# Performance work log

Measured on AMD Instinct MI355X. Metric: run time of the kernel, lower is better.

## Reference

```python
import jax, jax.numpy as jnp
import numpy as np

TIME_STEPS = 50
LEFT_PAD = 250 // TIME_STEPS            # 5
MAX_DELAY = LEFT_PAD if LEFT_PAD % 2 == 1 else LEFT_PAD + 1  # 5 (odd)
SIG = float(MAX_DELAY // 2)             # 2.0, frozen
CIN = 34 * 34 * 2                       # 2312
HID = 300
NOUT = 10
BETA = 0.9
THRESH = 1.0
BATCH = 128


def setup_inputs() -> dict:
    key = jax.random.key(0)
    k = jax.random.split(key, 6)
    data = jax.random.normal(k[0], (BATCH, TIME_STEPS, CIN), jnp.float32)
    W1 = jax.random.normal(k[1], (HID, CIN), jnp.float32) / np.sqrt(CIN * MAX_DELAY).astype(np.float32)
    P1 = jax.random.uniform(k[2], (HID, CIN), jnp.float32, -SIG, SIG)
    b1 = jnp.zeros((HID,), jnp.float32)
    W2 = jax.random.normal(k[3], (NOUT, HID), jnp.float32) / np.sqrt(HID * MAX_DELAY).astype(np.float32)
    P2 = jax.random.uniform(k[4], (NOUT, HID), jnp.float32, -SIG, SIG)
    b2 = jnp.zeros((NOUT,), jnp.float32)
    return {"data": data, "W1": W1, "P1": P1, "b1": b1, "W2": W2, "P2": P2, "b2": b2}


def make_gauss_kernel(W, P):
    # DCLS 'gauss': weight W placed at learnable position P (centered at KS//2)
    # with Gaussian of width SIG, normalized over the KS taps. kernel_count=1.
    idx = jnp.arange(MAX_DELAY, dtype=W.dtype)              # [KS]
    c = P[..., None] + (MAX_DELAY // 2)                     # [O, I, 1]
    g = jnp.exp(-0.5 * ((idx - c) / SIG) ** 2)              # [O, I, KS]
    g = g / (g.sum(-1, keepdims=True) + 1e-7)
    return W[..., None] * g                                 # [O, I, KS]


def delay_conv(x, W, P, b):
    # x: [B, Cin, L], valid conv with synthesized kernel -> [B, Cout, L-KS+1]
    K = make_gauss_kernel(W, P)
    y = jax.lax.conv_general_dilated(x, K, window_strides=(1,), padding='VALID',
                                     dimension_numbers=('NCH', 'OIH', 'NCH'))
    return y + b[None, :, None]


def lif_scan(x):
    # snntorch Leaky (reset-by-subtraction, reset detached):
    #   mem_t = beta*mem_{t-1} + x_t - H(mem_{t-1}-thr)*thr ;  spk_t = H(mem_t-thr)
    # x: [B, C, T] -> (spk [T,B,C], mem [T,B,C])
    def step(mem, xt):
        reset = (mem > THRESH).astype(xt.dtype)
        mem_new = BETA * mem + xt - reset * THRESH
        spk = (mem_new > THRESH).astype(xt.dtype)
        return mem_new, (spk, mem_new)

    xs = jnp.moveaxis(x, 2, 0)                              # [T, B, C]
    mem0 = jnp.zeros(x.shape[:2], x.dtype)
    _, (spks, mems) = jax.lax.scan(step, mem0, xs)
    return spks, mems


def reference(data, W1, P1, b1, W2, P2, b2):
    # pad time (dim -2) on the left, permute to [B, Cin, T+pad]
    x = jnp.pad(data, ((0, 0), (LEFT_PAD, 0), (0, 0)))
    x = jnp.transpose(x, (0, 2, 1))                         # [B, CIN, T+pad]
    x = delay_conv(x, W1, P1, b1)                           # [B, HID, T1]
    spk1, _ = lif_scan(x)                                   # [T1, B, HID]
    h = jnp.moveaxis(spk1, 0, 2)                            # [B, HID, T1]
    h = jnp.pad(h, ((0, 0), (0, 0), (LEFT_PAD, 0)))
    y = delay_conv(h, W2, P2, b2)                           # [B, NOUT, T2]
    spk2, mem2 = lif_scan(y)                                # [T2, B, NOUT] each
    return spk2, mem2
```

## Files before the change

### kernel.cpp

```cpp
#include <hip/hip_runtime.h>

#define BSZ  128
#define TT   50
#define CIN  2312
#define HID  300
#define NOUT 10
#define KS   5
#define T1   51
#define T2   52

#define NC32 73
#define KFRAG_U 20480

typedef unsigned int u32;
typedef unsigned short u16;
typedef __attribute__((ext_vector_type(8))) short s16x8;
typedef __attribute__((ext_vector_type(4))) float f32x4;

#define EK1f 0.88249690258459546f
#define EK2f 0.60653065971263342f
#define EK3f 0.32465246735834974f
#define EK4f 0.13533528323661270f

static __device__ __forceinline__ u16 bfhi(float x) {
  u32 u = __float_as_uint(x);
  return (u16)((u + 0x7fffu + ((u >> 16) & 1u)) >> 16);
}
static __device__ __forceinline__ float bf2f(u16 h) {
  return __uint_as_float(((u32)h) << 16);
}

__global__ __launch_bounds__(256) void snn_prepm(
    const float* __restrict__ W1, const float* __restrict__ P1,
    u16* __restrict__ K1bf)
{
  const int c  = blockIdx.x;
  const int ow = blockIdx.y;
  const int tid = threadIdx.x;
  const int nt = tid >> 6, ll = tid & 63;
  const int g = ll >> 4, lr = ll & 15;
  const int o  = ow * 64 + nt * 16 + lr;
  const int ib = c * 32 + g * 8;

  s16x8 hv[5], lv[5];
#pragma unroll
  for (int k = 0; k < 5; ++k)
#pragma unroll
    for (int j = 0; j < 8; ++j) { hv[k][j] = 0; lv[k][j] = 0; }

  if (o < HID) {
    const float* wrow = W1 + (size_t)o * CIN;
    const float* prow = P1 + (size_t)o * CIN;
#pragma unroll
    for (int j = 0; j < 8; ++j) {
      const int i = ib + j;
      if (i < CIN) {
        const float w1 = wrow[i], p1 = prow[i];
        const float cc = p1 + 2.0f;
        const float E0 = __expf(-0.125f * cc * cc);
        const float U  = __expf(0.25f * cc);
        const float u2 = U * U;
        const float e0 = E0;
        const float e1 = E0 * U * EK1f;
        const float e2 = E0 * u2 * EK2f;
        const float e3 = E0 * (u2 * U) * EK3f;
        const float e4 = E0 * (u2 * u2) * EK4f;
        const float inv = 1.0f / (((((e0 + e1) + e2) + e3) + e4) + 1e-7f);
        const float vk[5] = { w1 * (e0 * inv), w1 * (e1 * inv),
                              w1 * (e2 * inv), w1 * (e3 * inv),
                              w1 * (e4 * inv) };
#pragma unroll
        for (int k = 0; k < 5; ++k) {
          const u16 h = bfhi(vk[k]);
          const u16 lo = bfhi(vk[k] - bf2f(h));
          hv[k][j] = (short)h; lv[k][j] = (short)lo;
        }
      }
    }
  }
  u16* base = K1bf + ((size_t)ow * NC32 + c) * KFRAG_U + nt * 1024 + ll * 8;
#pragma unroll
  for (int k = 0; k < 5; ++k) {
    *(s16x8*)(base + k * 4096)       = hv[k];
    *(s16x8*)(base + k * 4096 + 512) = lv[k];
  }
}

__global__ __launch_bounds__(256, 2) void snn_l1m(
    const float* __restrict__ data, const u16* __restrict__ K1bf,
    const float* __restrict__ b1v, u32* __restrict__ gbits)
{
  __shared__ double dsm[3264];
  u16* A16 = (u16*)dsm;

  const int tid = threadIdx.x;
  const int bid = blockIdx.x;
  const int rnk = (bid & 7) * 80 + (bid >> 3);
  const int ow = rnk >> 7;
  const int b  = rnk & 127;

  const int w  = tid >> 6, l = tid & 63;
  const int lr = l & 15, lg = l >> 4;

  const float* dbase = data + (size_t)b * (TT * CIN);
  const u16* kbw = K1bf + (size_t)ow * NC32 * KFRAG_U + w * 1024 + l * 8;

  const int s1 = tid >> 2;
  const int j4 = tid & 3;
  const int tp = s1 - 5;
  const bool avld = (tp >= 0) && (tp < TT);
  const float* aptr = dbase + (size_t)(avld ? tp : 0) * CIN + j4 * 8;

  if (tid < 64) {
    s16x8 z;
#pragma unroll
    for (int j = 0; j < 8; ++j) z[j] = 0;
    const int r = tid >> 4, sub = tid & 15;
    const int row = 64 + (sub >> 2), off = (sub & 3) * 8;
    *(s16x8*)(A16 + (r >> 1) * 5440 + (r & 1) * 2720 + row * 40 + off) = z;
  }

  s16x8 bh0[5], bl0[5], bh1[5], bl1[5];

#define ISSUE_B(DH, DL, CC)                                                   \
  {                                                                           \
    const u16* cb_ = kbw + (size_t)(CC) * KFRAG_U;                            \
    _Pragma("unroll")                                                         \
    for (int k = 0; k < 5; ++k) {                                             \
      DH[k] = *(const s16x8*)(cb_ + k * 4096);                                \
      DL[k] = *(const s16x8*)(cb_ + k * 4096 + 512);                          \
    }                                                                         \
  }

#define STAGE_A(CC)                                                           \
  {                                                                           \
    const float f_[8] = { ra0.x, ra0.y, ra0.z, ra0.w,                         \
                          ra1.x, ra1.y, ra1.z, ra1.w };                       \
    s16x8 hv_, lv_;                                                           \
    _Pragma("unroll")                                                         \
    for (int j = 0; j < 8; ++j) {                                             \
      const u16 h_ = bfhi(f_[j]);                                             \
      hv_[j] = (short)h_;                                                     \
      lv_[j] = (short)bfhi(f_[j] - bf2f(h_));                                 \
    }                                                                         \
    u16* bn_ = A16 + (((CC) + 1) & 1) * 5440;                                 \
    const int woff_ = s1 * 40 + ((j4 * 8) ^ ((s1 & 3) << 3));                 \
    *(s16x8*)(bn_ + woff_) = hv_;                                             \
    *(s16x8*)(bn_ + 2720 + woff_) = lv_;                                      \
    const int cn_ = ((CC) + 2 <= 72) ? (CC) + 2 : 72;                         \
    const bool iv_ = avld && ((cn_ < 72) || (j4 == 0));                       \
    const float* pp_ = aptr + (size_t)cn_ * 32;                               \
    ra0 = iv_ ? *(const float4*)(pp_)     : make_float4(0.f, 0.f, 0.f, 0.f);  \
    ra1 = iv_ ? *(const float4*)(pp_ + 4) : make_float4(0.f, 0.f, 0.f, 0.f);  \
  }

#define COMPUTE(BH, BL, CC)                                                   \
  {                                                                           \
    const u16* bc_ = A16 + ((CC) & 1) * 5440;                                 \
    _Pragma("unroll")                                                         \
    for (int k = 0; k < 5; ++k) {                                             \
      const int xk_ = ((lr + k) & 3) << 3;                                    \
      const int a0_ = (lr + k) * 40 + ((lg * 8) ^ xk_);                       \
      _Pragma("unroll")                                                       \
      for (int m = 0; m < 4; ++m) {                                           \
        const s16x8 ah_ = *(const s16x8*)(bc_ + a0_ + m * 640);               \
        const s16x8 al_ = *(const s16x8*)(bc_ + 2720 + a0_ + m * 640);        \
        accf[m] = __builtin_amdgcn_mfma_f32_16x16x32_bf16(ah_, BH[k], accf[m], 0, 0, 0); \
        accf[m] = __builtin_amdgcn_mfma_f32_16x16x32_bf16(al_, BH[k], accf[m], 0, 0, 0); \
        accf[m] = __builtin_amdgcn_mfma_f32_16x16x32_bf16(ah_, BL[k], accf[m], 0, 0, 0); \
      }                                                                       \
    }                                                                         \
  }

#define PROMOTE()                                                             \
  _Pragma("unroll")                                                           \
  for (int m = 0; m < 4; ++m)                                                 \
    _Pragma("unroll")                                                         \
    for (int q = 0; q < 4; ++q) {                                             \
      accd[m][q] += (double)accf[m][q];                                       \
      accf[m][q] = 0.f;                                                       \
    }

  f32x4 accf[4];
  double accd[4][4];
#pragma unroll
  for (int m = 0; m < 4; ++m)
#pragma unroll
    for (int q = 0; q < 4; ++q) { accf[m][q] = 0.f; accd[m][q] = 0.0; }

  ISSUE_B(bh0, bl0, 0);
  float4 ra0, ra1;
  ra0 = avld ? *(const float4*)(aptr)     : make_float4(0.f, 0.f, 0.f, 0.f);
  ra1 = avld ? *(const float4*)(aptr + 4) : make_float4(0.f, 0.f, 0.f, 0.f);
  {
    const float f_[8] = { ra0.x, ra0.y, ra0.z, ra0.w,
                          ra1.x, ra1.y, ra1.z, ra1.w };
    s16x8 hv_, lv_;
#pragma unroll
    for (int j = 0; j < 8; ++j) {
      const u16 h_ = bfhi(f_[j]);
      hv_[j] = (short)h_;
      lv_[j] = (short)bfhi(f_[j] - bf2f(h_));
    }
    const int woff_ = s1 * 40 + ((j4 * 8) ^ ((s1 & 3) << 3));
    *(s16x8*)(A16 + woff_) = hv_;
    *(s16x8*)(A16 + 2720 + woff_) = lv_;
  }
  {
    const float* pp_ = aptr + 32;
    ra0 = avld ? *(const float4*)(pp_)     : make_float4(0.f, 0.f, 0.f, 0.f);
    ra1 = avld ? *(const float4*)(pp_ + 4) : make_float4(0.f, 0.f, 0.f, 0.f);
  }
  __syncthreads();

  for (int pr = 0; pr < 36; ++pr) {
    const int c0 = 2 * pr, c1 = c0 + 1;
    ISSUE_B(bh1, bl1, c0 + 1);
    STAGE_A(c0);
    COMPUTE(bh0, bl0, c0);
    __syncthreads();
    ISSUE_B(bh0, bl0, c1 + 1);
    STAGE_A(c1);
    COMPUTE(bh1, bl1, c1);
    PROMOTE();
    __syncthreads();
  }
  COMPUTE(bh0, bl0, 72);
  PROMOTE();
  __syncthreads();

#undef ISSUE_B
#undef STAGE_A
#undef COMPUTE
#undef PROMOTE

  double* y1s = dsm;
#pragma unroll
  for (int m = 0; m < 4; ++m)
#pragma unroll
    for (int q = 0; q < 4; ++q) {
      const int t = 16 * m + lg * 4 + q;
      if (t < T1) y1s[t * 64 + 16 * w + lr] = accd[m][q];
    }
  __syncthreads();

  if (tid < 64) {
    const int o = ow * 64 + tid;
    const bool valid = o < HID;
    const double bias = valid ? (double)b1v[o] : 0.0;
    u32* bits = gbits + (size_t)b * 510;
    double mem = 0.0;
    for (int t = 0; t < T1; ++t) {
      const double x = y1s[t * 64 + tid] + bias;
      const double reset = (mem > 1.0) ? 1.0 : 0.0;
      mem = __dsub_rn(__dadd_rn(__dmul_rn(0.9, mem), x), reset);
      const unsigned long long mk = __ballot(valid && (mem > 1.0));
      if (tid == 0)  bits[t * 10 + 2 * ow]     = (u32)mk;
      if (tid == 32) bits[t * 10 + 2 * ow + 1] = (u32)(mk >> 32);
    }
  }
}

__device__ __forceinline__ void layer1_tile_g(
    int b, int ow, int tid,
    const float* __restrict__ data, const float* __restrict__ W1,
    const float* __restrict__ P1, const float* __restrict__ b1v,
    double* __restrict__ dsm, u32* __restrict__ bits)
{
  float* Bsf = (float*)dsm;
  float* As  = (float*)dsm + 2880;

  const int ty = tid >> 5;
  const int tx = tid & 31;
  const int r0 = ty << 3;
  const int c0 = tx << 1;

  const float* abase = data + (size_t)b * (TT * CIN);

  const int slot = tid >> 2;
  const int pair = tid & 3;
  const int tp   = slot - 5;

  const int isub = tid & 7;
  const int oA = tid >> 3;
  const int oB = oA + 32;
  const int boA = ow * 64 + oA;
  const int boB = ow * 64 + oB;
  const bool vB = boB < HID;

  double acc[8][2];
#pragma unroll
  for (int r = 0; r < 8; ++r) { acc[r][0] = 0.0; acc[r][1] = 0.0; }

  float2 aA = make_float2(0.f, 0.f);
  float wA = 0.f, pA = 0.f, wB = 0.f, pB = 0.f;
  if (tid < 220 && tp >= 0)
    aA = *(const float2*)(abase + (size_t)tp * CIN + 2 * pair);
  wA = W1[(size_t)boA * CIN + isub];
  pA = P1[(size_t)boA * CIN + isub];
  if (vB) {
    wB = W1[(size_t)boB * CIN + isub];
    pB = P1[(size_t)boB * CIN + isub];
  }

  for (int i0 = 0; i0 < CIN; i0 += 8) {
    if (tid < 220) {
      As[(2 * pair) * 80 + slot]     = aA.x;
      As[(2 * pair + 1) * 80 + slot] = aA.y;
    }
    {
      const float c  = pA + 2.0f;
      const float E0 = __expf(-0.125f * c * c);
      const float U  = __expf(0.25f * c);
      const float u2 = U * U;
      const float e0 = E0;
      const float e1 = E0 * U * EK1f;
      const float e2 = E0 * u2 * EK2f;
      const float e3 = E0 * (u2 * U) * EK3f;
      const float e4 = E0 * (u2 * u2) * EK4f;
      const float inv = 1.0f / (((((e0 + e1) + e2) + e3) + e4) + 1e-7f);
      float* bp = Bsf + isub * 72 + oA;
      bp[0]    = wA * (e0 * inv);
      bp[576]  = wA * (e1 * inv);
      bp[1152] = wA * (e2 * inv);
      bp[1728] = wA * (e3 * inv);
      bp[2304] = wA * (e4 * inv);
    }
    {
      const float c  = pB + 2.0f;
      const float E0 = __expf(-0.125f * c * c);
      const float U  = __expf(0.25f * c);
      const float u2 = U * U;
      const float e0 = E0;
      const float e1 = E0 * U * EK1f;
      const float e2 = E0 * u2 * EK2f;
      const float e3 = E0 * (u2 * U) * EK3f;
      const float e4 = E0 * (u2 * u2) * EK4f;
      const float inv = 1.0f / (((((e0 + e1) + e2) + e3) + e4) + 1e-7f);
      float* bp = Bsf + isub * 72 + oB;
      bp[0]    = wB * (e0 * inv);
      bp[576]  = wB * (e1 * inv);
      bp[1152] = wB * (e2 * inv);
      bp[1728] = wB * (e3 * inv);
      bp[2304] = wB * (e4 * inv);
    }
    __syncthreads();

    const int i0n = i0 + 8;
    if (i0n < CIN) {
      if (tid < 220 && tp >= 0)
        aA = *(const float2*)(abase + (size_t)tp * CIN + i0n + 2 * pair);
      wA = W1[(size_t)boA * CIN + i0n + isub];
      pA = P1[(size_t)boA * CIN + i0n + isub];
      if (vB) {
        wB = W1[(size_t)boB * CIN + i0n + isub];
        pB = P1[(size_t)boB * CIN + i0n + isub];
      }
    }

    float accf[8][2];
#pragma unroll
    for (int r = 0; r < 8; ++r) { accf[r][0] = 0.f; accf[r][1] = 0.f; }
#pragma unroll
    for (int kk = 0; kk < 8; ++kk) {
      const float* ap = &As[kk * 80 + r0];
      const float4 a0 = *(const float4*)(ap);
      const float4 a1 = *(const float4*)(ap + 4);
      const float4 a2 = *(const float4*)(ap + 8);
      float av[12];
      av[0] = a0.x; av[1] = a0.y; av[2]  = a0.z; av[3]  = a0.w;
      av[4] = a1.x; av[5] = a1.y; av[6]  = a1.z; av[7]  = a1.w;
      av[8] = a2.x; av[9] = a2.y; av[10] = a2.z; av[11] = a2.w;
      float bv[KS][2];
#pragma unroll
      for (int k = 0; k < KS; ++k) {
        const float2 bb = *(const float2*)&Bsf[(k * 8 + kk) * 72 + c0];
        bv[k][0] = bb.x; bv[k][1] = bb.y;
      }
#pragma unroll
      for (int k = 0; k < KS; ++k)
#pragma unroll
        for (int r = 0; r < 8; ++r) {
          accf[r][0] = fmaf(av[r + k], bv[k][0], accf[r][0]);
          accf[r][1] = fmaf(av[r + k], bv[k][1], accf[r][1]);
        }
    }
#pragma unroll
    for (int r = 0; r < 8; ++r) {
      acc[r][0] += (double)accf[r][0];
      acc[r][1] += (double)accf[r][1];
    }
    __syncthreads();
  }

  double* y1s = dsm;
#pragma unroll
  for (int r = 0; r < 8; ++r) {
    const int t = r0 + r;
    if (t < T1) {
      y1s[t * 64 + c0]     = acc[r][0];
      y1s[t * 64 + c0 + 1] = acc[r][1];
    }
  }
  __syncthreads();

  if (tid < 64) {
    const int o = ow * 64 + tid;
    const bool valid = o < HID;
    const double bias = valid ? (double)b1v[o] : 0.0;
    double mem = 0.0;
    for (int t = 0; t < T1; ++t) {
      const double x = y1s[t * 64 + tid] + bias;
      const double reset = (mem > 1.0) ? 1.0 : 0.0;
      mem = __dsub_rn(__dadd_rn(__dmul_rn(0.9, mem), x), reset);
      const unsigned long long mk = __ballot(valid && (mem > 1.0));
      if (tid == 0)  bits[t * 10 + 2 * ow]     = (u32)mk;
      if (tid == 32) bits[t * 10 + 2 * ow + 1] = (u32)(mk >> 32);
    }
  }
  __syncthreads();
}

__device__ __forceinline__ void layer2_lif2(
    int b, int tid, float* smem,
    const float* __restrict__ W2, const float* __restrict__ P2,
    const float* __restrict__ b2, float* __restrict__ out)
{
  float* K2s = smem;
  const u32* lbits = (const u32*)(smem + 15000);
  float* y2s = smem + 15510;

  for (int idx = tid; idx < NOUT * HID; idx += 256) {
    const int o = idx / HID, i = idx % HID;
    const float w = W2[idx], p = P2[idx];
    const float c = p + 2.0f;
    float e[KS], s = 0.f;
#pragma unroll
    for (int k = 0; k < KS; ++k) {
      const float d = ((float)k - c) * 0.5f;
      e[k] = __expf(-0.5f * d * d);
      s += e[k];
    }
    const float denom = s + 1e-7f;
#pragma unroll
    for (int k = 0; k < KS; ++k)
      K2s[(o * KS + k) * HID + i] = w * (e[k] / denom);
  }
  __syncthreads();

  for (int task = tid; task < T2 * NOUT; task += 256) {
    const int t2 = task / NOUT, o = task % NOUT;
    float acc = b2[o];
#pragma unroll
    for (int k = 0; k < KS; ++k) {
      const int tp = t2 + k - KS;
      if (tp < 0 || tp >= T1) continue;
      const float* kr = K2s + (o * KS + k) * HID;
      const u32* br = lbits + tp * 10;
      for (int i = 0; i < HID; ++i)
        acc = fmaf((float)((br[i >> 5] >> (i & 31)) & 1u), kr[i], acc);
    }
    y2s[task] = acc;
  }
  __syncthreads();

  if (tid < NOUT) {
    float mem = 0.f;
    for (int t = 0; t < T2; ++t) {
      const float x = y2s[t * NOUT + tid];
      const float reset = (mem > 1.0f) ? 1.0f : 0.0f;
      mem = __fsub_rn(__fadd_rn(__fmul_rn(0.9f, mem), x), reset);
      out[(size_t)t * (BSZ * NOUT) + b * NOUT + tid] = (mem > 1.0f) ? 1.0f : 0.0f;
      out[(size_t)T2 * BSZ * NOUT + (size_t)t * (BSZ * NOUT) + b * NOUT + tid] = mem;
    }
  }
}

__global__ __launch_bounds__(256) void snn_l1(
    const float* __restrict__ data, const float* __restrict__ W1,
    const float* __restrict__ P1, const float* __restrict__ b1v,
    u32* __restrict__ gbits)
{
  __shared__ double dsm[3264];
  const int ow = blockIdx.x, b = blockIdx.y;
  layer1_tile_g(b, ow, threadIdx.x, data, W1, P1, b1v, dsm,
                gbits + (size_t)b * 510);
}

__global__ __launch_bounds__(256) void snn_l2k(
    const u32* __restrict__ gbits,
    const float* __restrict__ W2, const float* __restrict__ P2,
    const float* __restrict__ b2, float* __restrict__ out)
{
  __shared__ float smem[16030];
  const int b = blockIdx.x, tid = threadIdx.x;
  u32* lbits = (u32*)(smem + 15000);
  for (int i = tid; i < 510; i += 256) lbits[i] = gbits[(size_t)b * 510 + i];
  layer2_lif2(b, tid, smem, W2, P2, b2, out);
}

__global__ __launch_bounds__(256) void snn_mono(
    const float* __restrict__ data, const float* __restrict__ W1,
    const float* __restrict__ P1, const float* __restrict__ b1v,
    const float* __restrict__ W2, const float* __restrict__ P2,
    const float* __restrict__ b2, float* __restrict__ out)
{
  __shared__ double dsm[8015];
  const int b = blockIdx.x, tid = threadIdx.x;
  u32* lbits = (u32*)((float*)dsm + 15000);
  for (int ow = 0; ow < 5; ++ow)
    layer1_tile_g(b, ow, tid, data, W1, P1, b1v, dsm, lbits);
  layer2_lif2(b, tid, (float*)dsm, W2, P2, b2, out);
}

extern "C" void kernel_launch(void* const* d_in, const int* in_sizes, int n_in,
                              void* d_out, int out_size, void* d_ws, size_t ws_size,
                              hipStream_t stream) {
  const float* data = (const float*)d_in[0];
  const float* W1   = (const float*)d_in[1];
  const float* P1   = (const float*)d_in[2];
  const float* b1v  = (const float*)d_in[3];
  const float* W2   = (const float*)d_in[4];
  const float* P2   = (const float*)d_in[5];
  const float* b2   = (const float*)d_in[6];
  float* out = (float*)d_out;

  const size_t BITS_BYTES = (size_t)BSZ * T1 * 10 * sizeof(u32);
  const size_t K1_OFF = 262144;
  const size_t K1BF_BYTES = (size_t)5 * NC32 * KFRAG_U * 2;
  const size_t NEED_M = K1_OFF + K1BF_BYTES;

  if (ws_size >= NEED_M) {
    u32* gbits = (u32*)d_ws;
    u16* K1bf  = (u16*)((char*)d_ws + K1_OFF);
    snn_prepm<<<dim3(NC32, 5), 256, 0, stream>>>(W1, P1, K1bf);
    snn_l1m<<<640, 256, 0, stream>>>(data, K1bf, b1v, gbits);
    snn_l2k<<<BSZ, 256, 0, stream>>>(gbits, W2, P2, b2, out);
  } else if (ws_size >= BITS_BYTES) {
    u32* gbits = (u32*)d_ws;
    snn_l1<<<dim3(5, BSZ), 256, 0, stream>>>(data, W1, P1, b1v, gbits);
    snn_l2k<<<BSZ, 256, 0, stream>>>(gbits, W2, P2, b2, out);
  } else {
    snn_mono<<<BSZ, 256, 0, stream>>>(data, W1, P1, b1v, W2, P2, b2, out);
  }
}
```

Before: 463.8 us.

## Retile layer-1 MFMA into 2x2 wave grid with 4-stage LDS ring

Changes the wave tiling of the layer-1 delay-conv GEMM from four waves each covering all 64 time rows for one 16-column strip to a 2x2 grid where each wave covers 32 rows by 32 columns. This halves the A fragment LDS reads per wave but doubles the B register footprint. It also moves to a four-buffer LDS ring so two chunks are staged per barrier, with global loads issued two chunks ahead. B fragment reloads are interleaved per tap inside the MFMA loop. LDS grows and the XOR swizzle is dropped, which may bring back bank conflicts and raise register pressure under the two-blocks-per-CU launch bound.

```diff
diff --git a/kernel.cpp b/kernel.cpp
--- a/kernel.cpp
+++ b/kernel.cpp
@@ -90,7 +90,7 @@
     const float* __restrict__ data, const u16* __restrict__ K1bf,
     const float* __restrict__ b1v, u32* __restrict__ gbits)
 {
-  __shared__ double dsm[3264];
+  __shared__ __align__(16) double dsm[5440];
   u16* A16 = (u16*)dsm;
 
   const int tid = threadIdx.x;
@@ -101,9 +101,12 @@
 
   const int w  = tid >> 6, l = tid & 63;
   const int lr = l & 15, lg = l >> 4;
+  const int wr = w >> 1, wc = w & 1;
+  const int abase_u = (32 * wr + lr) * 40 + lg * 8;
 
   const float* dbase = data + (size_t)b * (TT * CIN);
-  const u16* kbw = K1bf + (size_t)ow * NC32 * KFRAG_U + w * 1024 + l * 8;
+  const u16* kbn = K1bf + (size_t)ow * NC32 * KFRAG_U + l * 8;
+  const int ntg0 = wc * 2, ntg1 = wc * 2 + 1;
 
   const int s1 = tid >> 2;
   const int j4 = tid & 3;
@@ -111,31 +114,37 @@
   const bool avld = (tp >= 0) && (tp < TT);
   const float* aptr = dbase + (size_t)(avld ? tp : 0) * CIN + j4 * 8;
 
-  if (tid < 64) {
+  if (tid < 160) {
     s16x8 z;
 #pragma unroll
     for (int j = 0; j < 8; ++j) z[j] = 0;
-    const int r = tid >> 4, sub = tid & 15;
-    const int row = 64 + (sub >> 2), off = (sub & 3) * 8;
-    *(s16x8*)(A16 + (r >> 1) * 5440 + (r & 1) * 2720 + row * 40 + off) = z;
-  }
-
-  s16x8 bh0[5], bl0[5], bh1[5], bl1[5];
-
-#define ISSUE_B(DH, DL, CC)                                                   \
+    const int buf = tid / 40, half = (tid / 20) & 1, off = (tid % 20) * 8;
+    *(s16x8*)(A16 + buf * 5440 + half * 2720 + 2560 + off) = z;
+  }
+
+  s16x8 bh[5][2], bl[5][2];
+#pragma unroll
+  for (int k = 0; k < 5; ++k) {
+    const u16* cb_ = kbn + k * 4096;
+    bh[k][0] = *(const s16x8*)(cb_ + ntg0 * 1024);
+    bh[k][1] = *(const s16x8*)(cb_ + ntg1 * 1024);
+    bl[k][0] = *(const s16x8*)(cb_ + ntg0 * 1024 + 512);
+    bl[k][1] = *(const s16x8*)(cb_ + ntg1 * 1024 + 512);
+  }
+
+#define LOADA(RA0, RA1, CC)                                                   \
   {                                                                           \
-    const u16* cb_ = kbw + (size_t)(CC) * KFRAG_U;                            \
-    _Pragma("unroll")                                                         \
-    for (int k = 0; k < 5; ++k) {                                             \
-      DH[k] = *(const s16x8*)(cb_ + k * 4096);                                \
-      DL[k] = *(const s16x8*)(cb_ + k * 4096 + 512);                          \
-    }                                                                         \
-  }
-
-#define STAGE_A(CC)                                                           \
-  {                                                                           \
-    const float f_[8] = { ra0.x, ra0.y, ra0.z, ra0.w,                         \
-                          ra1.x, ra1.y, ra1.z, ra1.w };                       \
+    const int cn_ = ((CC) <= 72) ? (CC) : 72;                                 \
+    const bool iv_ = avld && ((CC) <= 72) && ((cn_ < 72) || (j4 == 0));       \
+    const float* pp_ = aptr + (size_t)cn_ * 32;                               \
+    RA0 = iv_ ? *(const float4*)(pp_)     : make_float4(0.f, 0.f, 0.f, 0.f);  \
+    RA1 = iv_ ? *(const float4*)(pp_ + 4) : make_float4(0.f, 0.f, 0.f, 0.f);  \
+  }
+
+#define STAGE_A(CC, RA0, RA1)                                                 \
+  if ((CC) <= 72) {                                                           \
+    const float f_[8] = { RA0.x, RA0.y, RA0.z, RA0.w,                         \
+                          RA1.x, RA1.y, RA1.z, RA1.w };                       \
     s16x8 hv_, lv_;                                                           \
     _Pragma("unroll")                                                         \
     for (int j = 0; j < 8; ++j) {                                             \
@@ -143,105 +152,102 @@
       hv_[j] = (short)h_;                                                     \
       lv_[j] = (short)bfhi(f_[j] - bf2f(h_));                                 \
     }                                                                         \
-    u16* bn_ = A16 + (((CC) + 1) & 1) * 5440;                                 \
-    const int woff_ = s1 * 40 + ((j4 * 8) ^ ((s1 & 3) << 3));                 \
+    u16* bn_ = A16 + ((CC) & 3) * 5440;                                       \
+    const int woff_ = s1 * 40 + j4 * 8;                                       \
     *(s16x8*)(bn_ + woff_) = hv_;                                             \
     *(s16x8*)(bn_ + 2720 + woff_) = lv_;                                      \
-    const int cn_ = ((CC) + 2 <= 72) ? (CC) + 2 : 72;                         \
-    const bool iv_ = avld && ((cn_ < 72) || (j4 == 0));                       \
-    const float* pp_ = aptr + (size_t)cn_ * 32;                               \
-    ra0 = iv_ ? *(const float4*)(pp_)     : make_float4(0.f, 0.f, 0.f, 0.f);  \
-    ra1 = iv_ ? *(const float4*)(pp_ + 4) : make_float4(0.f, 0.f, 0.f, 0.f);  \
-  }
-
-#define COMPUTE(BH, BL, CC)                                                   \
+  }
+
+#define COMPUTE(CC, RC)                                                       \
   {                                                                           \
-    const u16* bc_ = A16 + ((CC) & 1) * 5440;                                 \
+    const u16* bc_ = A16 + ((CC) & 3) * 5440;                                 \
     _Pragma("unroll")                                                         \
     for (int k = 0; k < 5; ++k) {                                             \
-      const int xk_ = ((lr + k) & 3) << 3;                                    \
-      const int a0_ = (lr + k) * 40 + ((lg * 8) ^ xk_);                       \
-      _Pragma("unroll")                                                       \
-      for (int m = 0; m < 4; ++m) {                                           \
-        const s16x8 ah_ = *(const s16x8*)(bc_ + a0_ + m * 640);               \
-        const s16x8 al_ = *(const s16x8*)(bc_ + 2720 + a0_ + m * 640);        \
-        accf[m] = __builtin_amdgcn_mfma_f32_16x16x32_bf16(ah_, BH[k], accf[m], 0, 0, 0); \
-        accf[m] = __builtin_amdgcn_mfma_f32_16x16x32_bf16(al_, BH[k], accf[m], 0, 0, 0); \
-        accf[m] = __builtin_amdgcn_mfma_f32_16x16x32_bf16(ah_, BL[k], accf[m], 0, 0, 0); \
+      const s16x8 ah0 = *(const s16x8*)(bc_ + abase_u + k * 40);              \
+      const s16x8 al0 = *(const s16x8*)(bc_ + 2720 + abase_u + k * 40);       \
+      const s16x8 ah1 = *(const s16x8*)(bc_ + abase_u + (16 + k) * 40);       \
+      const s16x8 al1 = *(const s16x8*)(bc_ + 2720 + abase_u + (16 + k) * 40);\
+      accf[0][0] = __builtin_amdgcn_mfma_f32_16x16x32_bf16(ah0, bh[k][0], accf[0][0], 0, 0, 0); \
+      accf[0][0] = __builtin_amdgcn_mfma_f32_16x16x32_bf16(al0, bh[k][0], accf[0][0], 0, 0, 0); \
+      accf[0][0] = __builtin_amdgcn_mfma_f32_16x16x32_bf16(ah0, bl[k][0], accf[0][0], 0, 0, 0); \
+      accf[0][1] = __builtin_amdgcn_mfma_f32_16x16x32_bf16(ah0, bh[k][1], accf[0][1], 0, 0, 0); \
+      accf[0][1] = __builtin_amdgcn_mfma_f32_16x16x32_bf16(al0, bh[k][1], accf[0][1], 0, 0, 0); \
+      accf[0][1] = __builtin_amdgcn_mfma_f32_16x16x32_bf16(ah0, bl[k][1], accf[0][1], 0, 0, 0); \
+      accf[1][0] = __builtin_amdgcn_mfma_f32_16x16x32_bf16(ah1, bh[k][0], accf[1][0], 0, 0, 0); \
+      accf[1][0] = __builtin_amdgcn_mfma_f32_16x16x32_bf16(al1, bh[k][0], accf[1][0], 0, 0, 0); \
+      accf[1][0] = __builtin_amdgcn_mfma_f32_16x16x32_bf16(ah1, bl[k][0], accf[1][0], 0, 0, 0); \
+      accf[1][1] = __builtin_amdgcn_mfma_f32_16x16x32_bf16(ah1, bh[k][1], accf[1][1], 0, 0, 0); \
+      accf[1][1] = __builtin_amdgcn_mfma_f32_16x16x32_bf16(al1, bh[k][1], accf[1][1], 0, 0, 0); \
+      accf[1][1] = __builtin_amdgcn_mfma_f32_16x16x32_bf16(ah1, bl[k][1], accf[1][1], 0, 0, 0); \
+      if ((RC) <= 72) {                                                       \
+        const u16* cb_ = kbn + (size_t)(RC) * KFRAG_U + k * 4096;             \
+        bh[k][0] = *(const s16x8*)(cb_ + ntg0 * 1024);                        \
+        bh[k][1] = *(const s16x8*)(cb_ + ntg1 * 1024);                        \
+        bl[k][0] = *(const s16x8*)(cb_ + ntg0 * 1024 + 512);                  \
+        bl[k][1] = *(const s16x8*)(cb_ + ntg1 * 1024 + 512);                  \
       }                                                                       \
     }                                                                         \
   }
 
 #define PROMOTE()                                                             \
   _Pragma("unroll")                                                           \
-  for (int m = 0; m < 4; ++m)                                                 \
+  for (int m = 0; m < 2; ++m)                                                 \
     _Pragma("unroll")                                                         \
-    for (int q = 0; q < 4; ++q) {                                             \
-      accd[m][q] += (double)accf[m][q];                                       \
-      accf[m][q] = 0.f;                                                       \
-    }
-
-  f32x4 accf[4];
-  double accd[4][4];
-#pragma unroll
-  for (int m = 0; m < 4; ++m)
-#pragma unroll
-    for (int q = 0; q < 4; ++q) { accf[m][q] = 0.f; accd[m][q] = 0.0; }
-
-  ISSUE_B(bh0, bl0, 0);
-  float4 ra0, ra1;
-  ra0 = avld ? *(const float4*)(aptr)     : make_float4(0.f, 0.f, 0.f, 0.f);
-  ra1 = avld ? *(const float4*)(aptr + 4) : make_float4(0.f, 0.f, 0.f, 0.f);
-  {
-    const float f_[8] = { ra0.x, ra0.y, ra0.z, ra0.w,
-                          ra1.x, ra1.y, ra1.z, ra1.w };
-    s16x8 hv_, lv_;
-#pragma unroll
-    for (int j = 0; j < 8; ++j) {
-      const u16 h_ = bfhi(f_[j]);
-      hv_[j] = (short)h_;
-      lv_[j] = (short)bfhi(f_[j] - bf2f(h_));
-    }
-    const int woff_ = s1 * 40 + ((j4 * 8) ^ ((s1 & 3) << 3));
-    *(s16x8*)(A16 + woff_) = hv_;
-    *(s16x8*)(A16 + 2720 + woff_) = lv_;
-  }
-  {
-    const float* pp_ = aptr + 32;
-    ra0 = avld ? *(const float4*)(pp_)     : make_float4(0.f, 0.f, 0.f, 0.f);
-    ra1 = avld ? *(const float4*)(pp_ + 4) : make_float4(0.f, 0.f, 0.f, 0.f);
-  }
-  __syncthreads();
-
-  for (int pr = 0; pr < 36; ++pr) {
-    const int c0 = 2 * pr, c1 = c0 + 1;
-    ISSUE_B(bh1, bl1, c0 + 1);
-    STAGE_A(c0);
-    COMPUTE(bh0, bl0, c0);
-    __syncthreads();
-    ISSUE_B(bh0, bl0, c1 + 1);
-    STAGE_A(c1);
-    COMPUTE(bh1, bl1, c1);
+    for (int n = 0; n < 2; ++n)                                               \
+      _Pragma("unroll")                                                       \
+      for (int q = 0; q < 4; ++q) {                                           \
+        accd[m][n][q] += (double)accf[m][n][q];                               \
+        accf[m][n][q] = 0.f;                                                  \
+      }
+
+  f32x4 accf[2][2];
+  double accd[2][2][4];
+#pragma unroll
+  for (int m = 0; m < 2; ++m)
+#pragma unroll
+    for (int n = 0; n < 2; ++n)
+#pragma unroll
+      for (int q = 0; q < 4; ++q) { accf[m][n][q] = 0.f; accd[m][n][q] = 0.0; }
+
+  float4 raA0, raA1, raB0, raB1;
+  LOADA(raA0, raA1, 0);
+  LOADA(raB0, raB1, 1);
+  STAGE_A(0, raA0, raA1);
+  STAGE_A(1, raB0, raB1);
+  LOADA(raA0, raA1, 2);
+  LOADA(raB0, raB1, 3);
+  __syncthreads();
+
+  for (int pi = 0; pi < 36; ++pi) {
+    const int c0 = 2 * pi;
+    STAGE_A(c0 + 2, raA0, raA1);
+    STAGE_A(c0 + 3, raB0, raB1);
+    LOADA(raA0, raA1, c0 + 4);
+    LOADA(raB0, raB1, c0 + 5);
+    COMPUTE(c0,     c0 + 1);
+    COMPUTE(c0 + 1, c0 + 2);
     PROMOTE();
     __syncthreads();
   }
-  COMPUTE(bh0, bl0, 72);
+  COMPUTE(72, 73);
   PROMOTE();
   __syncthreads();
 
-#undef ISSUE_B
+#undef LOADA
 #undef STAGE_A
 #undef COMPUTE
 #undef PROMOTE
 
   double* y1s = dsm;
 #pragma unroll
-  for (int m = 0; m < 4; ++m)
-#pragma unroll
-    for (int q = 0; q < 4; ++q) {
-      const int t = 16 * m + lg * 4 + q;
-      if (t < T1) y1s[t * 64 + 16 * w + lr] = accd[m][q];
-    }
+  for (int m = 0; m < 2; ++m)
+#pragma unroll
+    for (int n = 0; n < 2; ++n)
+#pragma unroll
+      for (int q = 0; q < 4; ++q) {
+        const int t = 32 * wr + 16 * m + lg * 4 + q;
+        if (t < T1) y1s[t * 64 + 32 * wc + 16 * n + lr] = accd[m][n][q];
+      }
   __syncthreads();
 
   if (tid < 64) {
```

Measured after the change: 444.7 us. 4.1% less time.
